# Kernel tuning notes

Hardware: AMD Instinct MI355X
Metric: run time of the kernel (lower is better)

Reference implementation:

```python
import jax, jax.numpy as jnp
import numpy as np

N = 100000       # nodes
E = 1600000      # edges
EA = 7           # edge_attr_dim
H = 64           # hidden_dim
L = 32           # latent_dim
G = 512          # graphs in batch
C = 6            # num_classes


def _gin_conv(x, src, dst, edge_attr, We, be, W1, b1, W2, b2, eps):
    # GINE-style: message = relu(x_j + edge_proj), sum-aggregate at dst, then 2-layer MLP
    m = jax.nn.relu(x[src] + edge_attr @ We + be)            # [E, d_in]
    agg = jax.ops.segment_sum(m, dst, num_segments=x.shape[0])
    h = (1.0 + eps) * x + agg                                # [N, d_in]
    return jax.nn.relu(h @ W1 + b1) @ W2 + b2                # [N, H]


def setup_inputs() -> dict:
    key = jax.random.key(0)
    ks = jax.random.split(key, 24)
    s = 0.05
    inp = {
        "x": jax.random.normal(ks[0], (N,), jnp.float32),
        "edge_index": jax.random.randint(ks[1], (2, E), 0, N, jnp.int64),
        "edge_attr": jax.random.uniform(ks[2], (E, EA), jnp.float32),
        "batch": jnp.sort(jax.random.randint(ks[3], (N,), 0, G, jnp.int64)),
        # conv1 (input dim 1)
        "We1": jax.random.normal(ks[4], (EA, 1), jnp.float32) * s,
        "be1": jnp.zeros((1,), jnp.float32),
        "W11": jax.random.normal(ks[5], (1, H), jnp.float32) * s,
        "b11": jnp.zeros((H,), jnp.float32),
        "W12": jax.random.normal(ks[6], (H, H), jnp.float32) * s,
        "b12": jnp.zeros((H,), jnp.float32),
        "eps1": jnp.float32(0.0),
        # conv2 (input dim H)
        "We2": jax.random.normal(ks[7], (EA, H), jnp.float32) * s,
        "be2": jnp.zeros((H,), jnp.float32),
        "W21": jax.random.normal(ks[8], (H, H), jnp.float32) * s,
        "b21": jnp.zeros((H,), jnp.float32),
        "W22": jax.random.normal(ks[9], (H, H), jnp.float32) * s,
        "b22": jnp.zeros((H,), jnp.float32),
        "eps2": jnp.float32(0.0),
        # heads
        "Wmu": jax.random.normal(ks[10], (H, L), jnp.float32) * s,
        "bmu": jnp.zeros((L,), jnp.float32),
        "Wlv": jax.random.normal(ks[11], (H, L), jnp.float32) * s,
        "blv": jnp.zeros((L,), jnp.float32),
        "Wc": jax.random.normal(ks[12], (L, C), jnp.float32) * s,
        "bc": jnp.zeros((C,), jnp.float32),
    }
    return inp


def reference(x, edge_index, edge_attr, batch,
              We1, be1, W11, b11, W12, b12, eps1,
              We2, be2, W21, b21, W22, b22, eps2,
              Wmu, bmu, Wlv, blv, Wc, bc):
    src, dst = edge_index[0], edge_index[1]
    h = x.reshape(-1, 1)                                        # [N,1]
    h = jax.nn.relu(_gin_conv(h, src, dst, edge_attr, We1, be1, W11, b11, W12, b12, eps1))
    h = jax.nn.relu(_gin_conv(h, src, dst, edge_attr, We2, be2, W21, b21, W22, b22, eps2))
    mu = h @ Wmu + bmu                                          # [N,L]
    logvar = h @ Wlv + blv                                      # [N,L]
    # reparameterize (training path)
    noise = jax.random.normal(jax.random.key(42), mu.shape, mu.dtype)
    z = mu + noise * jnp.exp(0.5 * logvar)
    # global mean pool over graphs
    zsum = jax.ops.segment_sum(z, batch, num_segments=G)        # [G,L]
    cnt = jax.ops.segment_sum(jnp.ones((z.shape[0],), z.dtype), batch, num_segments=G)
    graph_emb = zsum / jnp.maximum(cnt, 1.0)[:, None]
    class_logits = graph_emb @ Wc + bc                          # [G,C]
    return (z, mu, logvar, class_logits)
```

## Files before the change

kernel.cpp:

```cpp
#include <hip/hip_runtime.h>
#include <stdint.h>

#define N_NODES 100000
#define N_EDGES 1600000
#define EAD 7
#define H 64
#define LAT 32
#define NG 512
#define NC 6
#define NZ (N_NODES * LAT)

#define NB_SCAN 391
#define NPW1 4
#define NPW2 2
#define C2_NPB 32
#define HD_NPB 8

static_assert(N_NODES % (4 * NPW1) == 0, "conv1 grid exact");
static_assert(N_NODES % (4 * NPW2) == 0, "conv2_agg grid exact");
static_assert(N_NODES % C2_NPB == 0, "conv2_node grid exact");
static_assert(N_NODES % HD_NPB == 0, "heads grid exact");
static_assert(N_EDGES % 256 == 0, "edge grid exact");

__device__ __forceinline__ void threefry2x32_42(uint32_t& x0, uint32_t& x1) {
    const uint32_t k0 = 0u, k1 = 42u;
    const uint32_t k2 = k0 ^ k1 ^ 0x1BD11BDAu;
    x0 += k0; x1 += k1;
#define TF_ROUND(r) { x0 += x1; x1 = (x1 << (r)) | (x1 >> (32 - (r))); x1 ^= x0; }
    TF_ROUND(13) TF_ROUND(15) TF_ROUND(26) TF_ROUND(6)
    x0 += k1; x1 += k2 + 1u;
    TF_ROUND(17) TF_ROUND(29) TF_ROUND(16) TF_ROUND(24)
    x0 += k2; x1 += k0 + 2u;
    TF_ROUND(13) TF_ROUND(15) TF_ROUND(26) TF_ROUND(6)
    x0 += k0; x1 += k1 + 3u;
    TF_ROUND(17) TF_ROUND(29) TF_ROUND(16) TF_ROUND(24)
    x0 += k1; x1 += k2 + 4u;
    TF_ROUND(13) TF_ROUND(15) TF_ROUND(26) TF_ROUND(6)
    x0 += k2; x1 += k0 + 5u;
#undef TF_ROUND
}

__device__ __forceinline__ float erfinv_f32(float x) {
    float w = -log1pf(-x * x);
    float p;
    if (w < 5.0f) {
        w = w - 2.5f;
        p = 2.81022636e-08f;
        p = fmaf(p, w, 3.43273939e-07f);
        p = fmaf(p, w, -3.5233877e-06f);
        p = fmaf(p, w, -4.39150654e-06f);
        p = fmaf(p, w, 0.00021858087f);
        p = fmaf(p, w, -0.00125372503f);
        p = fmaf(p, w, -0.00417768164f);
        p = fmaf(p, w, 0.246640727f);
        p = fmaf(p, w, 1.50140941f);
    } else {
        w = sqrtf(w) - 3.0f;
        p = -0.000200214257f;
        p = fmaf(p, w, 0.000100950558f);
        p = fmaf(p, w, 0.00134934322f);
        p = fmaf(p, w, -0.00367342844f);
        p = fmaf(p, w, 0.00573950773f);
        p = fmaf(p, w, -0.0076224613f);
        p = fmaf(p, w, 0.00943887047f);
        p = fmaf(p, w, 1.00167406f);
        p = fmaf(p, w, 2.83297682f);
    }
    return p * x;
}

__global__ void hist_k(const int* __restrict__ dst, int* __restrict__ deg) {
    int e = blockIdx.x * blockDim.x + threadIdx.x;
    if (e < N_EDGES) atomicAdd(&deg[dst[e]], 1);
}

__global__ void scan1_k(const int* __restrict__ deg, int* __restrict__ bsum) {
    __shared__ int sv[256];
    int t = threadIdx.x, i = blockIdx.x * 256 + t;
    sv[t] = (i < N_NODES) ? deg[i] : 0;
    __syncthreads();
    for (int o = 128; o > 0; o >>= 1) {
        if (t < o) sv[t] += sv[t + o];
        __syncthreads();
    }
    if (t == 0) bsum[blockIdx.x] = sv[0];
}

__global__ void scan2_k(int* __restrict__ bsum) {
    __shared__ int sv[512];
    int t = threadIdx.x;
    int v = (t < NB_SCAN) ? bsum[t] : 0;
    sv[t] = v;
    __syncthreads();
    for (int o = 1; o < 512; o <<= 1) {
        int a = (t >= o) ? sv[t - o] : 0;
        __syncthreads();
        sv[t] += a;
        __syncthreads();
    }
    if (t < NB_SCAN) bsum[t] = sv[t] - v;
}

__global__ void scan3_k(const int* __restrict__ deg, const int* __restrict__ bsum,
                        int* __restrict__ off, int* __restrict__ cur) {
    __shared__ int sv[256];
    int t = threadIdx.x, i = blockIdx.x * 256 + t;
    int v = (i < N_NODES) ? deg[i] : 0;
    sv[t] = v;
    __syncthreads();
    for (int o = 1; o < 256; o <<= 1) {
        int a = (t >= o) ? sv[t - o] : 0;
        __syncthreads();
        sv[t] += a;
        __syncthreads();
    }
    if (i < N_NODES) {
        int s = bsum[blockIdx.x] + sv[t] - v;
        off[i] = s;
        cur[i] = s;
    }
}

__global__ void scatter_k(const float* __restrict__ x, const int* __restrict__ src,
                          const int* __restrict__ dst, const float* __restrict__ ea,
                          const float* __restrict__ We1, const float* __restrict__ be1,
                          int* __restrict__ cur, int2* __restrict__ rec8,
                          float* __restrict__ m1s) {
    int e = blockIdx.x * blockDim.x + threadIdx.x;
    if (e >= N_EDGES) return;
    int s = src[e], d = dst[e];
    const float* ep = ea + (size_t)e * EAD;
    float p = be1[0];
#pragma unroll
    for (int k = 0; k < EAD; k++) p = fmaf(ep[k], We1[k], p);
    float m = x[s] + p;
    m = m > 0.0f ? m : 0.0f;
    int pos = atomicAdd(&cur[d], 1);
    rec8[pos] = make_int2(s, e);
    m1s[pos] = m;
}

__global__ void conv1_fused(const float* __restrict__ x, const float* __restrict__ m1s,
                            const int* __restrict__ off, const int* __restrict__ cur,
                            const float* __restrict__ W11, const float* __restrict__ b11,
                            const float* __restrict__ W12, const float* __restrict__ b12,
                            const float* __restrict__ eps1, float* __restrict__ hA) {
    __shared__ float sW12[H * H];
    __shared__ float stg[4][H];
    int tid = threadIdx.x;
    for (int i = tid; i < H * H; i += 256) sW12[i] = W12[i];
    int w = tid >> 6, lane = tid & 63;
    float rW11 = W11[lane], rb11 = b11[lane], rb12 = b12[lane], er = eps1[0];
    __syncthreads();
    int n0 = (blockIdx.x * 4 + w) * NPW1;
#pragma unroll
    for (int ni = 0; ni < NPW1; ni++) {
        int n = n0 + ni;
        int g0 = off[n], g1 = cur[n];
        float agg = 0.0f;
        for (int j = g0 + lane; j < g1; j += 64) agg += m1s[j];
#pragma unroll
        for (int o = 32; o > 0; o >>= 1) agg += __shfl_xor(agg, o, 64);
        float xv = x[n];
        float h1 = fmaf(er, xv, xv) + agg;
        float t = fmaf(h1, rW11, rb11);
        t = t > 0.0f ? t : 0.0f;
        stg[w][lane] = t;
        float acc = rb12;
#pragma unroll
        for (int j = 0; j < H; j++) acc = fmaf(stg[w][j], sW12[j * H + lane], acc);
        hA[(size_t)n * H + lane] = acc > 0.0f ? acc : 0.0f;
    }
}

__global__ void conv2_agg(const float* __restrict__ hin, const int2* __restrict__ rec8,
                          const float* __restrict__ ea,
                          const int* __restrict__ off, const int* __restrict__ cur,
                          const float* __restrict__ We2, const float* __restrict__ be2,
                          float4* __restrict__ agg4) {
    __shared__ float4 srec[4][64][2];
    __shared__ float stg[4][H];
    int tid = threadIdx.x;
    int w = tid >> 6, lane = tid & 63;
    float rW[EAD];
#pragma unroll
    for (int k = 0; k < EAD; k++) rW[k] = We2[k * H + lane];
    float rbe2 = be2[lane];

    int n0 = (blockIdx.x * 4 + w) * NPW2;
    int eend = cur[n0 + NPW2 - 1];
    int sbase = -(1 << 30);

    auto restage = [&](int g) {
        sbase = g;
        int cnt = eend - g; cnt = cnt > 64 ? 64 : cnt;
        float a0 = 0, a1 = 0, a2 = 0, a3 = 0, a4 = 0, a5 = 0, a6 = 0;
        int s = 0;
        if (lane < cnt) {
            int2 r = rec8[g + lane];
            s = r.x;
            const float* ep = ea + (size_t)r.y * EAD;
            a0 = ep[0]; a1 = ep[1]; a2 = ep[2]; a3 = ep[3];
            a4 = ep[4]; a5 = ep[5]; a6 = ep[6];
        }
        srec[w][lane][0] = make_float4(a0, a1, a2, a3);
        srec[w][lane][1] = make_float4(a4, a5, a6, __int_as_float(s));
    };

#pragma unroll
    for (int ni = 0; ni < NPW2; ni++) {
        int n = n0 + ni;
        int g = off[n], gend = cur[n];
        float acc = 0.0f;
        while (g + 4 <= gend) {
            if (g + 4 > sbase + 64) restage(g);
            int b = g - sbase;
            float4 A0 = srec[w][b + 0][0], B0 = srec[w][b + 0][1];
            float4 A1 = srec[w][b + 1][0], B1 = srec[w][b + 1][1];
            float4 A2 = srec[w][b + 2][0], B2 = srec[w][b + 2][1];
            float4 A3 = srec[w][b + 3][0], B3 = srec[w][b + 3][1];
            int s0 = __builtin_amdgcn_readfirstlane(__float_as_int(B0.w));
            int s1 = __builtin_amdgcn_readfirstlane(__float_as_int(B1.w));
            int s2 = __builtin_amdgcn_readfirstlane(__float_as_int(B2.w));
            int s3 = __builtin_amdgcn_readfirstlane(__float_as_int(B3.w));
            float hv0 = hin[(size_t)s0 * H + lane];
            float hv1 = hin[(size_t)s1 * H + lane];
            float hv2 = hin[(size_t)s2 * H + lane];
            float hv3 = hin[(size_t)s3 * H + lane];
            float p0 = rbe2, p1 = rbe2, p2 = rbe2, p3 = rbe2;
            p0 = fmaf(A0.x, rW[0], p0); p0 = fmaf(A0.y, rW[1], p0);
            p0 = fmaf(A0.z, rW[2], p0); p0 = fmaf(A0.w, rW[3], p0);
            p0 = fmaf(B0.x, rW[4], p0); p0 = fmaf(B0.y, rW[5], p0);
            p0 = fmaf(B0.z, rW[6], p0);
            p1 = fmaf(A1.x, rW[0], p1); p1 = fmaf(A1.y, rW[1], p1);
            p1 = fmaf(A1.z, rW[2], p1); p1 = fmaf(A1.w, rW[3], p1);
            p1 = fmaf(B1.x, rW[4], p1); p1 = fmaf(B1.y, rW[5], p1);
            p1 = fmaf(B1.z, rW[6], p1);
            p2 = fmaf(A2.x, rW[0], p2); p2 = fmaf(A2.y, rW[1], p2);
            p2 = fmaf(A2.z, rW[2], p2); p2 = fmaf(A2.w, rW[3], p2);
            p2 = fmaf(B2.x, rW[4], p2); p2 = fmaf(B2.y, rW[5], p2);
            p2 = fmaf(B2.z, rW[6], p2);
            p3 = fmaf(A3.x, rW[0], p3); p3 = fmaf(A3.y, rW[1], p3);
            p3 = fmaf(A3.z, rW[2], p3); p3 = fmaf(A3.w, rW[3], p3);
            p3 = fmaf(B3.x, rW[4], p3); p3 = fmaf(B3.y, rW[5], p3);
            p3 = fmaf(B3.z, rW[6], p3);
            acc += fmaxf(hv0 + p0, 0.0f);
            acc += fmaxf(hv1 + p1, 0.0f);
            acc += fmaxf(hv2 + p2, 0.0f);
            acc += fmaxf(hv3 + p3, 0.0f);
            g += 4;
        }
        while (g < gend) {
            if (g >= sbase + 64) restage(g);
            int b = g - sbase;
            float4 A = srec[w][b][0], B = srec[w][b][1];
            int s = __builtin_amdgcn_readfirstlane(__float_as_int(B.w));
            float hv = hin[(size_t)s * H + lane];
            float p = rbe2;
            p = fmaf(A.x, rW[0], p); p = fmaf(A.y, rW[1], p);
            p = fmaf(A.z, rW[2], p); p = fmaf(A.w, rW[3], p);
            p = fmaf(B.x, rW[4], p); p = fmaf(B.y, rW[5], p);
            p = fmaf(B.z, rW[6], p);
            acc += fmaxf(hv + p, 0.0f);
            g++;
        }
        stg[w][lane] = acc;
        if (lane < 16) {
            float4 v = make_float4(stg[w][lane * 4 + 0], stg[w][lane * 4 + 1],
                                   stg[w][lane * 4 + 2], stg[w][lane * 4 + 3]);
            agg4[(size_t)n * 16 + lane] = v;
        }
    }
}

__global__ void conv2_node(float* __restrict__ hA, const float* __restrict__ agg2,
                           const float* __restrict__ W21, const float* __restrict__ b21,
                           const float* __restrict__ W22, const float* __restrict__ b22,
                           const float* __restrict__ eps2) {
    __shared__ float sW21[H * H], sW22[H * H];
    __shared__ float sh2[4][H], st[4][H];
    int tid = threadIdx.x;
    for (int i = tid; i < H * H; i += 256) { sW21[i] = W21[i]; sW22[i] = W22[i]; }
    int sub = tid >> 6, lane = tid & 63;
    float e = eps2[0];
    float bb21 = b21[lane], bb22 = b22[lane];
    __syncthreads();
#pragma unroll
    for (int it = 0; it < C2_NPB / 4; it++) {
        int n = blockIdx.x * C2_NPB + it * 4 + sub;
        float hv = hA[(size_t)n * H + lane];
        sh2[sub][lane] = fmaf(e, hv, hv) + agg2[(size_t)n * H + lane];
        __syncthreads();
        float acc = bb21;
#pragma unroll
        for (int j = 0; j < H; j++) acc = fmaf(sh2[sub][j], sW21[j * H + lane], acc);
        st[sub][lane] = acc > 0.0f ? acc : 0.0f;
        __syncthreads();
        acc = bb22;
#pragma unroll
        for (int j = 0; j < H; j++) acc = fmaf(st[sub][j], sW22[j * H + lane], acc);
        hA[(size_t)n * H + lane] = acc > 0.0f ? acc : 0.0f;
        __syncthreads();
    }
}

__global__ void heads_fz2(const float* __restrict__ hA,
                          const float* __restrict__ Wmu, const float* __restrict__ bmu,
                          const float* __restrict__ Wlv, const float* __restrict__ blv,
                          float4* __restrict__ out4, float* __restrict__ zws) {
    __shared__ float sWmu[H * LAT], sWlv[H * LAT];
    __shared__ float sh[HD_NPB][H];
    __shared__ float sz[HD_NPB][LAT], smu[HD_NPB][LAT], slv[HD_NPB][LAT];
    int tid = threadIdx.x;
    for (int i = tid; i < H * LAT; i += 256) { sWmu[i] = Wmu[i]; sWlv[i] = Wlv[i]; }
    int sub = tid >> 5, lane = tid & 31;
    int base = blockIdx.x * HD_NPB;
#pragma unroll
    for (int i = tid; i < HD_NPB * H; i += 256)
        sh[i >> 6][i & 63] = hA[(size_t)(base + (i >> 6)) * H + (i & 63)];
    __syncthreads();
    int n = base + sub;
    float mu = bmu[lane], lv = blv[lane];
#pragma unroll
    for (int j = 0; j < H; j++) {
        float hv = sh[sub][j];
        mu = fmaf(hv, sWmu[j * LAT + lane], mu);
        lv = fmaf(hv, sWlv[j * LAT + lane], lv);
    }
    int i = n * LAT + lane;
    uint32_t x0 = 0u, x1 = (uint32_t)i;
    threefry2x32_42(x0, x1);
    uint32_t bits = x0 ^ x1;
    float f = __uint_as_float((bits >> 9) | 0x3F800000u) - 1.0f;
    const float lo = -0.99999994f;
    float u = fmaxf(lo, fmaf(f, 2.0f, lo));
    float noise = 1.41421356237309515f * erfinv_f32(u);
    float z = fmaf(noise, expf(0.5f * lv), mu);
    sz[sub][lane] = z; smu[sub][lane] = mu; slv[sub][lane] = lv;
    zws[i] = z;
    __syncthreads();
    if (tid < 192) {
        int grp = tid >> 6;
        int q = tid & 63;
        int nl = q >> 3, f4 = q & 7;
        const float* s = (grp == 0) ? &sz[0][0] : (grp == 1) ? &smu[0][0] : &slv[0][0];
        float4 v = ((const float4*)s)[q];
        out4[(size_t)grp * (NZ / 4) + (size_t)(base + nl) * 8 + f4] = v;
    }
}

__global__ void pool_logits_k(const float4* __restrict__ z4, const int* __restrict__ batch,
                              const float* __restrict__ Wc, const float* __restrict__ bc,
                              float* __restrict__ out) {
    int g = blockIdx.x;
    int tid = threadIdx.x;
    int sub = tid >> 3, slot = tid & 7;
    __shared__ float4 acc4[32][8];
    __shared__ float emb[LAT];
    int lo = 0, hi = N_NODES;
    while (lo < hi) { int mid = (lo + hi) >> 1; if (batch[mid] < g) lo = mid + 1; else hi = mid; }
    int start = lo;
    hi = N_NODES;
    while (lo < hi) { int mid = (lo + hi) >> 1; if (batch[mid] < g + 1) lo = mid + 1; else hi = mid; }
    int end = lo;
    float4 a = make_float4(0.f, 0.f, 0.f, 0.f);
    for (int n = start + sub; n < end; n += 32) {
        float4 v = z4[(size_t)n * (LAT / 4) + slot];
        a.x += v.x; a.y += v.y; a.z += v.z; a.w += v.w;
    }
    acc4[sub][slot] = a;
    __syncthreads();
    if (tid < 8) {
        float4 s4 = acc4[0][tid];
        for (int k = 1; k < 32; k++) {
            s4.x += acc4[k][tid].x; s4.y += acc4[k][tid].y;
            s4.z += acc4[k][tid].z; s4.w += acc4[k][tid].w;
        }
        float invc = 1.0f / fmaxf((float)(end - start), 1.0f);
        emb[tid * 4 + 0] = s4.x * invc; emb[tid * 4 + 1] = s4.y * invc;
        emb[tid * 4 + 2] = s4.z * invc; emb[tid * 4 + 3] = s4.w * invc;
    }
    __syncthreads();
    if (tid < NC) {
        float r = bc[tid];
#pragma unroll
        for (int l = 0; l < LAT; l++) r = fmaf(emb[l], Wc[l * NC + tid], r);
        out[g * NC + tid] = r;
    }
}

extern "C" void kernel_launch(void* const* d_in, const int* in_sizes, int n_in,
                              void* d_out, int out_size, void* d_ws, size_t ws_size,
                              hipStream_t stream) {
    const float* x     = (const float*)d_in[0];
    const int*   ei    = (const int*)d_in[1];
    const float* ea    = (const float*)d_in[2];
    const int*   batch = (const int*)d_in[3];
    const float* We1   = (const float*)d_in[4];
    const float* be1   = (const float*)d_in[5];
    const float* W11   = (const float*)d_in[6];
    const float* b11   = (const float*)d_in[7];
    const float* W12   = (const float*)d_in[8];
    const float* b12   = (const float*)d_in[9];
    const float* eps1  = (const float*)d_in[10];
    const float* We2   = (const float*)d_in[11];
    const float* be2   = (const float*)d_in[12];
    const float* W21   = (const float*)d_in[13];
    const float* b21   = (const float*)d_in[14];
    const float* W22   = (const float*)d_in[15];
    const float* b22   = (const float*)d_in[16];
    const float* eps2  = (const float*)d_in[17];
    const float* Wmu   = (const float*)d_in[18];
    const float* bmu   = (const float*)d_in[19];
    const float* Wlv   = (const float*)d_in[20];
    const float* blv   = (const float*)d_in[21];
    const float* Wc    = (const float*)d_in[22];
    const float* bc    = (const float*)d_in[23];

    int*   deg  = (int*)d_ws;
    int*   off  = deg + N_NODES;
    int*   cur  = off + N_NODES;
    int*   bsum = cur + N_NODES;
    int2*  rec8 = (int2*)(bsum + 512);
    float* m1s  = (float*)(rec8 + N_EDGES);
    float* hA   = m1s + N_EDGES;
    float* zws  = (float*)rec8;
    float* agg2 = (float*)d_out;
    float* outf = (float*)d_out;

    hipMemsetAsync(deg, 0, N_NODES * sizeof(int), stream);

    const int* src = ei;
    const int* dst = ei + N_EDGES;

    hist_k<<<N_EDGES / 256, 256, 0, stream>>>(dst, deg);
    scan1_k<<<NB_SCAN, 256, 0, stream>>>(deg, bsum);
    scan2_k<<<1, 512, 0, stream>>>(bsum);
    scan3_k<<<NB_SCAN, 256, 0, stream>>>(deg, bsum, off, cur);
    scatter_k<<<N_EDGES / 256, 256, 0, stream>>>(x, src, dst, ea, We1, be1, cur, rec8, m1s);
    conv1_fused<<<N_NODES / (4 * NPW1), 256, 0, stream>>>(
        x, m1s, off, cur, W11, b11, W12, b12, eps1, hA);
    conv2_agg<<<N_NODES / (4 * NPW2), 256, 0, stream>>>(
        hA, rec8, ea, off, cur, We2, be2, (float4*)agg2);
    conv2_node<<<N_NODES / C2_NPB, 256, 0, stream>>>(hA, agg2, W21, b21, W22, b22, eps2);
    heads_fz2<<<N_NODES / HD_NPB, 256, 0, stream>>>(
        hA, Wmu, bmu, Wlv, blv, (float4*)outf, zws);
    pool_logits_k<<<NG, 256, 0, stream>>>((const float4*)zws, batch, Wc, bc,
                                          outf + 3 * (size_t)NZ);
}
```

Before: 864.9 us.

## Fuse conv2 edge aggregation with node MLP into one kernel

Adds conv2_fused, which aggregates edge messages per node and immediately applies both 64x64 MLP layers in the same wave. This removes the agg2 round trip through global memory and one kernel launch. Because hA cannot be overwritten in place while other nodes still read it, the output goes to a separate hB buffer. The fused path is taken only when the workspace is large enough, otherwise the old two-kernel path runs. It also changes heads to write z to the workspace as float4 vectors. Risks include extra shared memory for two weight matrices per block, which lowers occupancy, and per-block weight reloads.

```diff
diff --git a/kernel.cpp b/kernel.cpp
--- a/kernel.cpp
+++ b/kernel.cpp
@@ -13,11 +13,13 @@
 #define NB_SCAN 391
 #define NPW1 4
 #define NPW2 2
+#define NPW2F 2
 #define C2_NPB 32
 #define HD_NPB 8
 
 static_assert(N_NODES % (4 * NPW1) == 0, "conv1 grid exact");
 static_assert(N_NODES % (4 * NPW2) == 0, "conv2_agg grid exact");
+static_assert(N_NODES % (4 * NPW2F) == 0, "conv2_fused grid exact");
 static_assert(N_NODES % C2_NPB == 0, "conv2_node grid exact");
 static_assert(N_NODES % HD_NPB == 0, "heads grid exact");
 static_assert(N_EDGES % 256 == 0, "edge grid exact");
@@ -170,6 +172,117 @@
 #pragma unroll
         for (int j = 0; j < H; j++) acc = fmaf(stg[w][j], sW12[j * H + lane], acc);
         hA[(size_t)n * H + lane] = acc > 0.0f ? acc : 0.0f;
+    }
+}
+
+__global__ void conv2_fused(const float* __restrict__ hin, const int2* __restrict__ rec8,
+                            const float* __restrict__ ea,
+                            const int* __restrict__ off, const int* __restrict__ cur,
+                            const float* __restrict__ We2, const float* __restrict__ be2,
+                            const float* __restrict__ W21, const float* __restrict__ b21,
+                            const float* __restrict__ W22, const float* __restrict__ b22,
+                            const float* __restrict__ eps2, float* __restrict__ hB) {
+    __shared__ float sW21[H * H], sW22[H * H];
+    __shared__ float4 srec[4][64][2];
+    __shared__ float stg[4][H];
+    int tid = threadIdx.x;
+    for (int i = tid; i < H * H; i += 256) { sW21[i] = W21[i]; sW22[i] = W22[i]; }
+    int w = tid >> 6, lane = tid & 63;
+    float rW[EAD];
+#pragma unroll
+    for (int k = 0; k < EAD; k++) rW[k] = We2[k * H + lane];
+    float rbe2 = be2[lane], rb21 = b21[lane], rb22 = b22[lane], er = eps2[0];
+    __syncthreads();
+
+    int n0 = (blockIdx.x * 4 + w) * NPW2F;
+    int eend = cur[n0 + NPW2F - 1];
+    int sbase = -(1 << 30);
+
+    auto restage = [&](int g) {
+        sbase = g;
+        int cnt = eend - g; cnt = cnt > 64 ? 64 : cnt;
+        float a0 = 0, a1 = 0, a2 = 0, a3 = 0, a4 = 0, a5 = 0, a6 = 0;
+        int s = 0;
+        if (lane < cnt) {
+            int2 r = rec8[g + lane];
+            s = r.x;
+            const float* ep = ea + (size_t)r.y * EAD;
+            a0 = ep[0]; a1 = ep[1]; a2 = ep[2]; a3 = ep[3];
+            a4 = ep[4]; a5 = ep[5]; a6 = ep[6];
+        }
+        srec[w][lane][0] = make_float4(a0, a1, a2, a3);
+        srec[w][lane][1] = make_float4(a4, a5, a6, __int_as_float(s));
+    };
+
+#pragma unroll
+    for (int ni = 0; ni < NPW2F; ni++) {
+        int n = n0 + ni;
+        int g = off[n], gend = cur[n];
+        float acc = 0.0f;
+        while (g + 4 <= gend) {
+            if (g + 4 > sbase + 64) restage(g);
+            int b = g - sbase;
+            float4 A0 = srec[w][b + 0][0], B0 = srec[w][b + 0][1];
+            float4 A1 = srec[w][b + 1][0], B1 = srec[w][b + 1][1];
+            float4 A2 = srec[w][b + 2][0], B2 = srec[w][b + 2][1];
+            float4 A3 = srec[w][b + 3][0], B3 = srec[w][b + 3][1];
+            int s0 = __builtin_amdgcn_readfirstlane(__float_as_int(B0.w));
+            int s1 = __builtin_amdgcn_readfirstlane(__float_as_int(B1.w));
+            int s2 = __builtin_amdgcn_readfirstlane(__float_as_int(B2.w));
+            int s3 = __builtin_amdgcn_readfirstlane(__float_as_int(B3.w));
+            float hv0 = hin[(size_t)s0 * H + lane];
+            float hv1 = hin[(size_t)s1 * H + lane];
+            float hv2 = hin[(size_t)s2 * H + lane];
+            float hv3 = hin[(size_t)s3 * H + lane];
+            float p0 = rbe2, p1 = rbe2, p2 = rbe2, p3 = rbe2;
+            p0 = fmaf(A0.x, rW[0], p0); p0 = fmaf(A0.y, rW[1], p0);
+            p0 = fmaf(A0.z, rW[2], p0); p0 = fmaf(A0.w, rW[3], p0);
+            p0 = fmaf(B0.x, rW[4], p0); p0 = fmaf(B0.y, rW[5], p0);
+            p0 = fmaf(B0.z, rW[6], p0);
+            p1 = fmaf(A1.x, rW[0], p1); p1 = fmaf(A1.y, rW[1], p1);
+            p1 = fmaf(A1.z, rW[2], p1); p1 = fmaf(A1.w, rW[3], p1);
+            p1 = fmaf(B1.x, rW[4], p1); p1 = fmaf(B1.y, rW[5], p1);
+            p1 = fmaf(B1.z, rW[6], p1);
+            p2 = fmaf(A2.x, rW[0], p2); p2 = fmaf(A2.y, rW[1], p2);
+            p2 = fmaf(A2.z, rW[2], p2); p2 = fmaf(A2.w, rW[3], p2);
+            p2 = fmaf(B2.x, rW[4], p2); p2 = fmaf(B2.y, rW[5], p2);
+            p2 = fmaf(B2.z, rW[6], p2);
+            p3 = fmaf(A3.x, rW[0], p3); p3 = fmaf(A3.y, rW[1], p3);
+            p3 = fmaf(A3.z, rW[2], p3); p3 = fmaf(A3.w, rW[3], p3);
+            p3 = fmaf(B3.x, rW[4], p3); p3 = fmaf(B3.y, rW[5], p3);
+            p3 = fmaf(B3.z, rW[6], p3);
+            acc += fmaxf(hv0 + p0, 0.0f);
+            acc += fmaxf(hv1 + p1, 0.0f);
+            acc += fmaxf(hv2 + p2, 0.0f);
+            acc += fmaxf(hv3 + p3, 0.0f);
+            g += 4;
+        }
+        while (g < gend) {
+            if (g >= sbase + 64) restage(g);
+            int b = g - sbase;
+            float4 A = srec[w][b][0], B = srec[w][b][1];
+            int s = __builtin_amdgcn_readfirstlane(__float_as_int(B.w));
+            float hv = hin[(size_t)s * H + lane];
+            float p = rbe2;
+            p = fmaf(A.x, rW[0], p); p = fmaf(A.y, rW[1], p);
+            p = fmaf(A.z, rW[2], p); p = fmaf(A.w, rW[3], p);
+            p = fmaf(B.x, rW[4], p); p = fmaf(B.y, rW[5], p);
+            p = fmaf(B.z, rW[6], p);
+            acc += fmaxf(hv + p, 0.0f);
+            g++;
+        }
+        float hself = hin[(size_t)n * H + lane];
+        float h2 = fmaf(er, hself, hself) + acc;
+        stg[w][lane] = h2;
+        float t = rb21;
+#pragma unroll
+        for (int j = 0; j < H; j++) t = fmaf(stg[w][j], sW21[j * H + lane], t);
+        t = t > 0.0f ? t : 0.0f;
+        stg[w][lane] = t;
+        float o2 = rb22;
+#pragma unroll
+        for (int j = 0; j < H; j++) o2 = fmaf(stg[w][j], sW22[j * H + lane], o2);
+        hB[(size_t)n * H + lane] = o2 > 0.0f ? o2 : 0.0f;
     }
 }
 
@@ -304,10 +417,10 @@
     }
 }
 
-__global__ void heads_fz2(const float* __restrict__ hA,
+__global__ void heads_fz2(const float* __restrict__ hsrc,
                           const float* __restrict__ Wmu, const float* __restrict__ bmu,
                           const float* __restrict__ Wlv, const float* __restrict__ blv,
-                          float4* __restrict__ out4, float* __restrict__ zws) {
+                          float4* __restrict__ out4, float4* __restrict__ zws4) {
     __shared__ float sWmu[H * LAT], sWlv[H * LAT];
     __shared__ float sh[HD_NPB][H];
     __shared__ float sz[HD_NPB][LAT], smu[HD_NPB][LAT], slv[HD_NPB][LAT];
@@ -317,7 +430,7 @@
     int base = blockIdx.x * HD_NPB;
 #pragma unroll
     for (int i = tid; i < HD_NPB * H; i += 256)
-        sh[i >> 6][i & 63] = hA[(size_t)(base + (i >> 6)) * H + (i & 63)];
+        sh[i >> 6][i & 63] = hsrc[(size_t)(base + (i >> 6)) * H + (i & 63)];
     __syncthreads();
     int n = base + sub;
     float mu = bmu[lane], lv = blv[lane];
@@ -337,7 +450,6 @@
     float noise = 1.41421356237309515f * erfinv_f32(u);
     float z = fmaf(noise, expf(0.5f * lv), mu);
     sz[sub][lane] = z; smu[sub][lane] = mu; slv[sub][lane] = lv;
-    zws[i] = z;
     __syncthreads();
     if (tid < 192) {
         int grp = tid >> 6;
@@ -346,6 +458,7 @@
         const float* s = (grp == 0) ? &sz[0][0] : (grp == 1) ? &smu[0][0] : &slv[0][0];
         float4 v = ((const float4*)s)[q];
         out4[(size_t)grp * (NZ / 4) + (size_t)(base + nl) * 8 + f4] = v;
+        if (grp == 0) zws4[(size_t)base * 8 + q] = v;
     }
 }
 
@@ -424,9 +537,13 @@
     int2*  rec8 = (int2*)(bsum + 512);
     float* m1s  = (float*)(rec8 + N_EDGES);
     float* hA   = m1s + N_EDGES;
+    float* hB   = hA + (size_t)N_NODES * H;
     float* zws  = (float*)rec8;
-    float* agg2 = (float*)d_out;
     float* outf = (float*)d_out;
+
+    const size_t PATHA_BYTES =
+        (size_t)(3 * N_NODES + 512) * 4 + (size_t)N_EDGES * 12 +
+        2 * (size_t)N_NODES * H * 4;
 
     hipMemsetAsync(deg, 0, N_NODES * sizeof(int), stream);
 
@@ -440,11 +557,20 @@
     scatter_k<<<N_EDGES / 256, 256, 0, stream>>>(x, src, dst, ea, We1, be1, cur, rec8, m1s);
     conv1_fused<<<N_NODES / (4 * NPW1), 256, 0, stream>>>(
         x, m1s, off, cur, W11, b11, W12, b12, eps1, hA);
-    conv2_agg<<<N_NODES / (4 * NPW2), 256, 0, stream>>>(
-        hA, rec8, ea, off, cur, We2, be2, (float4*)agg2);
-    conv2_node<<<N_NODES / C2_NPB, 256, 0, stream>>>(hA, agg2, W21, b21, W22, b22, eps2);
-    heads_fz2<<<N_NODES / HD_NPB, 256, 0, stream>>>(
-        hA, Wmu, bmu, Wlv, blv, (float4*)outf, zws);
+
+    if (ws_size >= PATHA_BYTES) {
+        conv2_fused<<<N_NODES / (4 * NPW2F), 256, 0, stream>>>(
+            hA, rec8, ea, off, cur, We2, be2, W21, b21, W22, b22, eps2, hB);
+        heads_fz2<<<N_NODES / HD_NPB, 256, 0, stream>>>(
+            hB, Wmu, bmu, Wlv, blv, (float4*)outf, (float4*)zws);
+    } else {
+        float* agg2 = (float*)d_out;
+        conv2_agg<<<N_NODES / (4 * NPW2), 256, 0, stream>>>(
+            hA, rec8, ea, off, cur, We2, be2, (float4*)agg2);
+        conv2_node<<<N_NODES / C2_NPB, 256, 0, stream>>>(hA, agg2, W21, b21, W22, b22, eps2);
+        heads_fz2<<<N_NODES / HD_NPB, 256, 0, stream>>>(
+            hA, Wmu, bmu, Wlv, blv, (float4*)outf, (float4*)zws);
+    }
     pool_logits_k<<<NG, 256, 0, stream>>>((const float4*)zws, batch, Wc, bc,
                                           outf + 3 * (size_t)NZ);
 }
```

After: 864.3 us. No clear change (-0.1%).
